# Optimization experiments

Hardware: AMD Instinct MI355X
Metric: run time of the kernel (lower is better)

Reference implementation:

```python
import jax, jax.numpy as jnp
import numpy as np

EPS = 1.1920929e-7  # torch.finfo(float32).eps, default for F.rms_norm
ATTN_SCALE = 0.1
ROPE_BASE = 10000.0


def _rms_norm(x):
    # F.rms_norm over last dim, no learned weight
    return x * jax.lax.rsqrt(jnp.mean(x * x, axis=-1, keepdims=True) + EPS)


def _rotary(x):
    # x: [B, T, H, D]; rotates halves as in the Rotary module
    T, D = x.shape[1], x.shape[3]
    half = D // 2
    inv_freq = 1.0 / (ROPE_BASE ** (jnp.arange(0, D, 2, dtype=jnp.float32) / D))  # [half]
    freqs = jnp.arange(T, dtype=jnp.float32)[:, None] * inv_freq[None, :]          # [T, half]
    cos = jnp.cos(freqs)[None, :, None, :]
    sin = jnp.sin(freqs)[None, :, None, :]
    x1, x2 = x[..., :half], x[..., half:]
    return jnp.concatenate([x1 * cos + x2 * sin, -x1 * sin + x2 * cos], axis=-1)


def setup_inputs() -> dict:
    key = jax.random.key(0)
    ks = jax.random.split(key, 8)
    B, T, dim, H, hd = 2, 2048, 1024, 16, 64
    gate_in = 12
    s = 1.0 / np.sqrt(dim)
    return {
        "x": jax.random.normal(ks[0], (B, T, dim), dtype=jnp.float32),
        "v1": jax.random.normal(ks[1], (B, T, H, hd), dtype=jnp.float32),
        "Wq": jax.random.uniform(ks[2], (dim, dim), jnp.float32, -s, s),
        "Wk": jax.random.uniform(ks[3], (dim, dim), jnp.float32, -s, s),
        "Wv": jax.random.uniform(ks[4], (dim, dim), jnp.float32, -s, s),
        "Wproj": jax.random.uniform(ks[5], (dim, dim), jnp.float32, -s, s),
        "Wg": jax.random.uniform(ks[6], (H, gate_in), jnp.float32,
                                  -1.0 / np.sqrt(gate_in), 1.0 / np.sqrt(gate_in)),
        "lamb": jnp.float32(0.5),
    }


def reference(x, v1, Wq, Wk, Wv, Wproj, Wg, lamb):
    B, T, dim = x.shape
    H, hd = v1.shape[2], v1.shape[3]
    q = (x @ Wq.T).reshape(B, T, H, hd)
    k = (x @ Wk.T).reshape(B, T, H, hd)
    v = (x @ Wv.T).reshape(B, T, H, hd)
    # value-residual mixing
    v = (1.0 - lamb) * v + lamb * v1
    # QK RMSNorm + RoPE
    q = _rotary(_rms_norm(q))
    k = _rotary(_rms_norm(k))
    # causal SDPA with fixed scale
    scores = jnp.einsum('bqhd,bkhd->bhqk', q, k) * ATTN_SCALE
    causal = jnp.tril(jnp.ones((T, T), dtype=bool))
    scores = jnp.where(causal[None, None], scores, jnp.float32(-jnp.inf))
    probs = jax.nn.softmax(scores, axis=-1)
    y = jnp.einsum('bhqk,bkhd->bqhd', probs, v)  # [B, T, H, hd]
    # sigmoid gate from first 12 channels of x
    gate = jax.nn.sigmoid(x[..., :Wg.shape[1]] @ Wg.T)  # [B, T, H]
    y = y * gate[..., None]
    y = y.reshape(B, T, H * hd) @ Wproj.T
    return y
```

## Files before the change

kernel.cpp:

```cpp
#include <hip/hip_runtime.h>
#include <math.h>


#define B_    2
#define T_    2048
#define DIM_  1024
#define H_    16
#define HD_   64
#define NROW  (B_ * T_)
#define EPS_  1.1920929e-07f
#define SCALE_ 0.1f
#define LOG2_10K 13.287712379549449f
#define INV2PI 0.15915494309189535f

typedef unsigned short u16;
typedef unsigned int   u32;
typedef __bf16 bf16x8 __attribute__((ext_vector_type(8)));
typedef __bf16 bf16x2 __attribute__((ext_vector_type(2)));
typedef float  f32x4  __attribute__((ext_vector_type(4)));

__device__ __forceinline__ u16 f2b(float f) {
  u32 u = __float_as_uint(f);
  u += 0x7fffu + ((u >> 16) & 1u);
  return (u16)(u >> 16);
}
__device__ __forceinline__ u32 pk2(float a, float b) {
#if __has_builtin(__builtin_amdgcn_cvt_pk_bf16_f32)
  bf16x2 r = __builtin_amdgcn_cvt_pk_bf16_f32(a, b);
  return __builtin_bit_cast(u32, r);
#else
  return (u32)f2b(a) | ((u32)f2b(b) << 16);
#endif
}
__device__ __forceinline__ void fast_sincos_rev(float rev, float* s, float* c) {
  const float r = rev - floorf(rev);
#if __has_builtin(__builtin_amdgcn_sinf) && __has_builtin(__builtin_amdgcn_cosf)
  *s = __builtin_amdgcn_sinf(r);
  *c = __builtin_amdgcn_cosf(r);
#else
  *s = __sinf(r * 6.283185307179586f);
  *c = __cosf(r * 6.283185307179586f);
#endif
}
#define MFMA16(a,b,c) __builtin_amdgcn_mfma_f32_16x16x32_bf16((a),(b),(c),0,0,0)

typedef const __attribute__((address_space(1))) unsigned char gbuf_t;
typedef __attribute__((address_space(3))) unsigned char lbuf_t;
__device__ __forceinline__ void gload_lds16(const u16* g, unsigned char* l) {
  __builtin_amdgcn_global_load_lds((gbuf_t*)g, (lbuf_t*)l, 16, 0, 0);
}

__global__ __launch_bounds__(256) void convert_all(
    const float* __restrict__ x, const float* __restrict__ Wq,
    const float* __restrict__ Wk, const float* __restrict__ Wv,
    const float* __restrict__ Wp,
    u16* __restrict__ xb, u16* __restrict__ wb ) {
  const int i = blockIdx.x * 256 + threadIdx.x;
  const float* src;
  u16* dst;
  int off;
  if (i < 1048576)       { src = x;  dst = xb;            off = i; }
  else if (i < 1310720)  { src = Wq; dst = wb;            off = i - 1048576; }
  else if (i < 1572864)  { src = Wk; dst = wb + 1048576;  off = i - 1310720; }
  else if (i < 1835008)  { src = Wv; dst = wb + 2097152;  off = i - 1572864; }
  else                   { src = Wp; dst = wb + 3145728;  off = i - 1835008; }
  const float4 f = ((const float4*)src)[off];
  uint2 o;
  o.x = pk2(f.x, f.y);
  o.y = pk2(f.z, f.w);
  ((uint2*)dst)[off] = o;
}

template <bool IS_PROJ>
__global__ __launch_bounds__(256) void gemm_rp(
    const u16* __restrict__ Ab, const u16* __restrict__ Wb,
    u16* __restrict__ qo, u16* __restrict__ ko, u16* __restrict__ vto,
    float* __restrict__ fo, const float* __restrict__ v1,
    const float* __restrict__ lambp) {
  __shared__ __attribute__((aligned(16))) unsigned char sm[49152];
  const int tid  = threadIdx.x;
  const int w    = tid >> 6;
  const int lane = tid & 63;
  const int lo = lane & 15, hi = lane >> 4;
  const int m0 = blockIdx.x << 7;
  const int by = blockIdx.y;
  const int mode = IS_PROJ ? 3 : (by >> 3);
  const int n0 = IS_PROJ ? (by << 7) : ((by & 7) << 7);
  const u16* W = IS_PROJ ? Wb : (Wb + (size_t)mode * (DIM_ * DIM_));

  const int wm = w & 1, wn = w >> 1;

  const u16* agA0 = Ab + (size_t)(m0 + (2 * w + 0) * 16 + lo) * DIM_ + (hi << 3);
  const u16* agA1 = Ab + (size_t)(m0 + (2 * w + 1) * 16 + lo) * DIM_ + (hi << 3);
  const u16* agB0 = W  + (size_t)(n0 + (2 * w + 0) * 16 + lo) * DIM_ + (hi << 3);
  const u16* agB1 = W  + (size_t)(n0 + (2 * w + 1) * 16 + lo) * DIM_ + (hi << 3);

  f32x4 acc[4][4];
#pragma unroll
  for (int i = 0; i < 4; ++i)
#pragma unroll
    for (int j = 0; j < 4; ++j) acc[i][j] = (f32x4){0.f, 0.f, 0.f, 0.f};

  {
    unsigned char* ad0 = sm + (2 * w) * 1024;
    gload_lds16(agA0, ad0);
    gload_lds16(agA1, ad0 + 1024);
    gload_lds16(agB0, ad0 + 8192);
    gload_lds16(agB1, ad0 + 9216);
    agA0 += 32; agA1 += 32; agB0 += 32; agB1 += 32;
    unsigned char* ad1 = sm + 16384 + (2 * w) * 1024;
    gload_lds16(agA0, ad1);
    gload_lds16(agA1, ad1 + 1024);
    gload_lds16(agB0, ad1 + 8192);
    gload_lds16(agB1, ad1 + 9216);
    agA0 += 32; agA1 += 32; agB0 += 32; agB1 += 32;
  }

  int cr = 0;
  int cw = 2;
  for (int kc = 0; kc < DIM_; kc += 32) {
    __builtin_amdgcn_sched_barrier(0);
    if (kc + 32 < DIM_) {
      asm volatile("s_waitcnt vmcnt(4)" ::: "memory");
    } else {
      asm volatile("s_waitcnt vmcnt(0)" ::: "memory");
    }
    __builtin_amdgcn_s_barrier();
    __builtin_amdgcn_sched_barrier(0);
    if (kc + 64 < DIM_) {
      unsigned char* ad = sm + cw * 16384 + (2 * w) * 1024;
      gload_lds16(agA0, ad);
      gload_lds16(agA1, ad + 1024);
      gload_lds16(agB0, ad + 8192);
      gload_lds16(agB1, ad + 9216);
      agA0 += 32; agA1 += 32; agB0 += 32; agB1 += 32;
    }
    const unsigned char* Acur = sm + cr * 16384;
    const unsigned char* Bcur = Acur + 8192;
    bf16x8 bfr[4];
#pragma unroll
    for (int nt = 0; nt < 4; ++nt)
      bfr[nt] = *(const bf16x8*)(Bcur + (((wn * 4 + nt) * 64 + lane) << 4));
#pragma unroll
    for (int mt = 0; mt < 4; ++mt) {
      const bf16x8 af = *(const bf16x8*)(Acur + (((wm * 4 + mt) * 64 + lane) << 4));
#pragma unroll
      for (int nt = 0; nt < 4; ++nt)
        acc[mt][nt] = MFMA16(af, bfr[nt], acc[mt][nt]);
    }
    cr = (cr == 2) ? 0 : cr + 1;
    cw = (cw == 2) ? 0 : cw + 1;
  }

  const int head = (n0 >> 6) + wn;
  if (mode <= 1) {
    u16* C = (mode == 0) ? qo : ko;
    const float if0 = exp2f(-(float)lo * (LOG2_10K / 32.f)) * INV2PI;
    const float if1 = exp2f(-(float)(lo + 16) * (LOG2_10K / 32.f)) * INV2PI;
#pragma unroll
    for (int mt = 0; mt < 4; ++mt)
#pragma unroll
      for (int r = 0; r < 4; ++r) {
        float ss = 0.f;
#pragma unroll
        for (int nt = 0; nt < 4; ++nt) { const float v = acc[mt][nt][r]; ss += v * v; }
        ss += __shfl_xor(ss, 1, 64); ss += __shfl_xor(ss, 2, 64);
        ss += __shfl_xor(ss, 4, 64); ss += __shfl_xor(ss, 8, 64);
        const float scl = rsqrtf(ss * (1.f / 64.f) + EPS_);
        const int row_g = m0 + wm * 64 + mt * 16 + hi * 4 + r;
        const float tpos = (float)(row_g & (T_ - 1));
        float sn0, cs0, sn1, cs1;
        fast_sincos_rev(tpos * if0, &sn0, &cs0);
        fast_sincos_rev(tpos * if1, &sn1, &cs1);
        u16* crow = C + (size_t)row_g * DIM_ + head * HD_;
        const float x10 = acc[mt][0][r] * scl, x11 = acc[mt][1][r] * scl;
        const float x20 = acc[mt][2][r] * scl, x21 = acc[mt][3][r] * scl;
        crow[lo]      = f2b(x10 * cs0 + x20 * sn0);
        crow[16 + lo] = f2b(x11 * cs1 + x21 * sn1);
        crow[32 + lo] = f2b(x20 * cs0 - x10 * sn0);
        crow[48 + lo] = f2b(x21 * cs1 - x11 * sn1);
      }
  } else if (mode == 2) {
    const float lam = lambp[0];
#pragma unroll
    for (int mt = 0; mt < 4; ++mt)
#pragma unroll
      for (int r = 0; r < 4; ++r) {
        const int row_g = m0 + wm * 64 + mt * 16 + hi * 4 + r;
        const int bb = row_g >> 11, tt = row_g & (T_ - 1);
        const int bh = bb * H_ + head;
        const float* v1r = v1 + (size_t)row_g * DIM_ + head * HD_;
#pragma unroll
        for (int nt = 0; nt < 4; ++nt) {
          const int d = nt * 16 + lo;
          const float ov = (1.f - lam) * acc[mt][nt][r] + lam * v1r[d];
          vto[((size_t)(bh * HD_ + d)) * T_ + tt] = f2b(ov);
        }
      }
  } else {
#pragma unroll
    for (int mt = 0; mt < 4; ++mt)
#pragma unroll
      for (int r = 0; r < 4; ++r) {
        const int row_g = m0 + wm * 64 + mt * 16 + hi * 4 + r;
        float* orow = fo + (size_t)row_g * DIM_ + n0 + wn * 64;
#pragma unroll
        for (int nt = 0; nt < 4; ++nt) orow[nt * 16 + lo] = acc[mt][nt][r];
      }
  }
}

__global__ __launch_bounds__(256) void gate_kernel(
    const float* __restrict__ x, const float* __restrict__ Wg,
    float* __restrict__ gate) {
  const int id = blockIdx.x * 256 + threadIdx.x;
  const int n = id >> 4, h = id & 15;
  const float* xr = x + (size_t)n * DIM_;
  const float* wr = Wg + h * 12;
  float s = 0.f;
#pragma unroll
  for (int j = 0; j < 12; ++j) s += xr[j] * wr[j];
  gate[id] = 1.f / (1.f + __expf(-s));
}

__global__ __launch_bounds__(256) void attn3(
    const u16* __restrict__ q, const u16* __restrict__ k, const u16* __restrict__ vt,
    const float* __restrict__ gate, u16* __restrict__ y) {
  __shared__ __attribute__((aligned(16))) unsigned char smem[16384];
  const int tid = threadIdx.x;
  const int wv = tid >> 6, lane = tid & 63, lo = lane & 15, hi = lane >> 4;
  const int idx = blockIdx.x;
  const int qt = 31 - (idx >> 5);
  const int bh = idx & 31;
  const int b = bh >> 4, h = bh & 15;
  const int qb = qt << 6;

  const int qrow = b * T_ + qb + wv * 16 + lo;
  const u16* qp = q + (size_t)qrow * DIM_ + h * HD_;
  const bf16x8 qf0 = *(const bf16x8*)(qp + hi * 8);
  const bf16x8 qf1 = *(const bf16x8*)(qp + 32 + hi * 8);

  f32x4 o[4];
#pragma unroll
  for (int i = 0; i < 4; ++i) o[i] = (f32x4){0.f, 0.f, 0.f, 0.f};
  float lrun = 0.f;

  const int sl = tid & 63, skh = (tid >> 6) & 1, st0 = tid >> 7;
  const int srow = sl & 15, skk = skh * 32 + ((sl >> 4) << 3);
  const u16* kg0 = k + ((size_t)(b * T_ + st0 * 16 + srow)) * DIM_ + h * HD_ + skk;
  const u16* kg1 = kg0 + (size_t)32 * DIM_;
  const u16* vg0 = vt + ((size_t)(bh * HD_ + st0 * 16 + srow)) * T_ + skk;
  const u16* vg1 = vg0 + (size_t)32 * T_;

  uint4 kr0 = *(const uint4*)kg0, kr1 = *(const uint4*)kg1;
  uint4 vr0 = *(const uint4*)vg0, vr1 = *(const uint4*)vg1;

  const int off0 = tid << 4, off1 = (tid + 256) << 4;

  for (int tix = 0; tix <= qt; ++tix) {
    __syncthreads();
    *(uint4*)(smem + off0) = kr0;
    *(uint4*)(smem + off1) = kr1;
    *(uint4*)(smem + 8192 + off0) = vr0;
    *(uint4*)(smem + 8192 + off1) = vr1;
    if (tix < qt) {
      const size_t ko = (size_t)(tix + 1) * 64 * DIM_;
      const size_t vo = (size_t)(tix + 1) * 64;
      kr0 = *(const uint4*)(kg0 + ko); kr1 = *(const uint4*)(kg1 + ko);
      vr0 = *(const uint4*)(vg0 + vo); vr1 = *(const uint4*)(vg1 + vo);
    }
    __syncthreads();

    f32x4 stl[4];
#pragma unroll
    for (int kt = 0; kt < 4; ++kt) stl[kt] = (f32x4){0.f, 0.f, 0.f, 0.f};
    __builtin_amdgcn_s_setprio(1);
#pragma unroll
    for (int kh = 0; kh < 2; ++kh) {
      const bf16x8 qb_ = kh ? qf1 : qf0;
#pragma unroll
      for (int kt = 0; kt < 4; ++kt) {
        const bf16x8 af = *(const bf16x8*)(smem + (((kt * 2 + kh) * 64 + lane) << 4));
        stl[kt] = MFMA16(af, qb_, stl[kt]);
      }
    }
    __builtin_amdgcn_s_setprio(0);
    const bool diag = (tix == qt);
    float ps = 0.f;
#pragma unroll
    for (int kt = 0; kt < 4; ++kt)
#pragma unroll
      for (int r = 0; r < 4; ++r) {
        float s = stl[kt][r] * SCALE_;
        if (diag && (kt * 16 + hi * 4 + r > wv * 16 + lo)) s = -3e38f;
        const float e = __expf(s);
        stl[kt][r] = e;
        ps += e;
      }
    ps += __shfl_xor(ps, 16, 64);
    ps += __shfl_xor(ps, 32, 64);
    lrun += ps;

    u32 pkv[4][2];
#pragma unroll
    for (int kt = 0; kt < 4; ++kt) {
      pkv[kt][0] = pk2(stl[kt][0], stl[kt][1]);
      pkv[kt][1] = pk2(stl[kt][2], stl[kt][3]);
    }
#pragma unroll
    for (int kh = 0; kh < 2; ++kh) {
      uint4 w4;
      u32* w4p = (u32*)&w4;
#pragma unroll
      for (int wd = 0; wd < 4; ++wd) {
        const int src = (2 * (hi & 1) + (wd >> 1)) * 16 + lo;
        const u32 a  = (u32)__shfl((int)pkv[2 * kh][wd & 1], src, 64);
        const u32 bb = (u32)__shfl((int)pkv[2 * kh + 1][wd & 1], src, 64);
        w4p[wd] = (hi < 2) ? a : bb;
      }
      const bf16x8 pf = __builtin_bit_cast(bf16x8, w4);
      __builtin_amdgcn_s_setprio(1);
#pragma unroll
      for (int dt = 0; dt < 4; ++dt) {
        const bf16x8 vf = *(const bf16x8*)(smem + 8192 + (((dt * 2 + kh) * 64 + lane) << 4));
        o[dt] = MFMA16(vf, pf, o[dt]);
      }
      __builtin_amdgcn_s_setprio(0);
    }
  }

  const float inv = gate[(size_t)qrow * H_ + h] / lrun;
  u16* yrow = y + (size_t)qrow * DIM_ + h * HD_;
#pragma unroll
  for (int dt = 0; dt < 4; ++dt) {
    ushort4 pq;
    pq.x = f2b(o[dt][0] * inv); pq.y = f2b(o[dt][1] * inv);
    pq.z = f2b(o[dt][2] * inv); pq.w = f2b(o[dt][3] * inv);
    *(ushort4*)(yrow + dt * 16 + hi * 4) = pq;
  }
}

extern "C" void kernel_launch(void* const* d_in, const int* in_sizes, int n_in,
                              void* d_out, int out_size, void* d_ws, size_t ws_size,
                              hipStream_t stream) {
  const float* x    = (const float*)d_in[0];
  const float* v1   = (const float*)d_in[1];
  const float* Wq   = (const float*)d_in[2];
  const float* Wk   = (const float*)d_in[3];
  const float* Wv   = (const float*)d_in[4];
  const float* Wp   = (const float*)d_in[5];
  const float* Wg   = (const float*)d_in[6];
  const float* lamb = (const float*)d_in[7];

  const size_t NX = (size_t)NROW * DIM_;
  const size_t NW = (size_t)DIM_ * DIM_;

  u16* q  = (u16*)d_ws;
  u16* k  = q + NX;
  u16* vt = k + NX;
  u16* xb = vt + NX;
  u16* wb = xb + NX;
  float* gate = (float*)(wb + 4 * NW);

  const dim3 bb(256);

  convert_all<<<dim3(8192), bb, 0, stream>>>(x, Wq, Wk, Wv, Wp, xb, wb);
  gemm_rp<false><<<dim3(NROW / 128, 24), bb, 0, stream>>>(
      xb, wb, q, k, vt, nullptr, v1, lamb);
  gate_kernel<<<dim3(NROW * H_ / 256), bb, 0, stream>>>(x, Wg, gate);
  attn3<<<dim3(B_ * H_ * (T_ / 64)), bb, 0, stream>>>(q, k, vt, gate, q);
  gemm_rp<true><<<dim3(NROW / 128, 8), bb, 0, stream>>>(
      q, wb + 3 * NW, nullptr, nullptr, nullptr, (float*)d_out, nullptr, nullptr);
}
```

Before: 221.3 us.

## Triple-buffer attention K/V via direct-to-LDS loads and XCD-aware block remap

The attention kernel now streams K/V tiles with direct global-to-LDS loads into a three-stage ring buffer. It prefetches two tiles ahead and uses explicit vmcnt waits with a single barrier per iteration, replacing register staging and two barriers. Both GEMM and attention grids are flattened and remapped so consecutive blocks on the same XCD share A rows or the same batch-head, aiming for better L2 locality. LDS use in attention triples to 48KB, which may reduce occupancy.

New measurement: 221.0 us. No clear change (-0.1%).

```diff
diff --git a/kernel.cpp b/kernel.cpp
--- a/kernel.cpp
+++ b/kernel.cpp
@@ -82,8 +82,11 @@
   const int w    = tid >> 6;
   const int lane = tid & 63;
   const int lo = lane & 15, hi = lane >> 4;
-  const int m0 = blockIdx.x << 7;
-  const int by = blockIdx.y;
+  const int raw = blockIdx.x;
+  const int xcd = raw & 7;
+  const int jj  = raw >> 3;
+  const int m0 = (xcd * 4 + (jj & 3)) << 7;
+  const int by = jj >> 2;
   const int mode = IS_PROJ ? 3 : (by >> 3);
   const int n0 = IS_PROJ ? (by << 7) : ((by & 7) << 7);
   const u16* W = IS_PROJ ? Wb : (Wb + (size_t)mode * (DIM_ * DIM_));
@@ -226,12 +229,14 @@
 __global__ __launch_bounds__(256) void attn3(
     const u16* __restrict__ q, const u16* __restrict__ k, const u16* __restrict__ vt,
     const float* __restrict__ gate, u16* __restrict__ y) {
-  __shared__ __attribute__((aligned(16))) unsigned char smem[16384];
+  __shared__ __attribute__((aligned(16))) unsigned char smem[49152];
   const int tid = threadIdx.x;
   const int wv = tid >> 6, lane = tid & 63, lo = lane & 15, hi = lane >> 4;
-  const int idx = blockIdx.x;
-  const int qt = 31 - (idx >> 5);
-  const int bh = idx & 31;
+  const int raw = blockIdx.x;
+  const int xcd = raw & 7;
+  const int jj  = raw >> 3;
+  const int qt = 31 - (jj >> 2);
+  const int bh = xcd * 4 + (jj & 3);
   const int b = bh >> 4, h = bh & 15;
   const int qb = qt << 6;
 
@@ -251,25 +256,44 @@
   const u16* kg1 = kg0 + (size_t)32 * DIM_;
   const u16* vg0 = vt + ((size_t)(bh * HD_ + st0 * 16 + srow)) * T_ + skk;
   const u16* vg1 = vg0 + (size_t)32 * T_;
-
-  uint4 kr0 = *(const uint4*)kg0, kr1 = *(const uint4*)kg1;
-  uint4 vr0 = *(const uint4*)vg0, vr1 = *(const uint4*)vg1;
-
-  const int off0 = tid << 4, off1 = (tid + 256) << 4;
-
+  const int wub = (tid >> 6) << 10;
+
+  {
+    gload_lds16(kg0, smem + wub);
+    gload_lds16(kg1, smem + 4096 + wub);
+    gload_lds16(vg0, smem + 8192 + wub);
+    gload_lds16(vg1, smem + 12288 + wub);
+    const int t1 = (qt >= 1) ? 1 : 0;
+    const size_t ko = (size_t)t1 * 64 * DIM_;
+    const size_t vo = (size_t)t1 * 64;
+    unsigned char* b1 = smem + 16384;
+    gload_lds16(kg0 + ko, b1 + wub);
+    gload_lds16(kg1 + ko, b1 + 4096 + wub);
+    gload_lds16(vg0 + vo, b1 + 8192 + wub);
+    gload_lds16(vg1 + vo, b1 + 12288 + wub);
+  }
+
+  int sr = 0, sw = 2;
   for (int tix = 0; tix <= qt; ++tix) {
-    __syncthreads();
-    *(uint4*)(smem + off0) = kr0;
-    *(uint4*)(smem + off1) = kr1;
-    *(uint4*)(smem + 8192 + off0) = vr0;
-    *(uint4*)(smem + 8192 + off1) = vr1;
+    __builtin_amdgcn_sched_barrier(0);
     if (tix < qt) {
-      const size_t ko = (size_t)(tix + 1) * 64 * DIM_;
-      const size_t vo = (size_t)(tix + 1) * 64;
-      kr0 = *(const uint4*)(kg0 + ko); kr1 = *(const uint4*)(kg1 + ko);
-      vr0 = *(const uint4*)(vg0 + vo); vr1 = *(const uint4*)(vg1 + vo);
-    }
-    __syncthreads();
+      asm volatile("s_waitcnt vmcnt(4)" ::: "memory");
+    } else {
+      asm volatile("s_waitcnt vmcnt(0)" ::: "memory");
+    }
+    __builtin_amdgcn_s_barrier();
+    __builtin_amdgcn_sched_barrier(0);
+    if (tix + 2 <= qt) {
+      const size_t ko = (size_t)(tix + 2) * 64 * DIM_;
+      const size_t vo = (size_t)(tix + 2) * 64;
+      unsigned char* base = smem + sw * 16384;
+      gload_lds16(kg0 + ko, base + wub);
+      gload_lds16(kg1 + ko, base + 4096 + wub);
+      gload_lds16(vg0 + vo, base + 8192 + wub);
+      gload_lds16(vg1 + vo, base + 12288 + wub);
+    }
+    const unsigned char* kb = smem + sr * 16384;
+    const unsigned char* vb = kb + 8192;
 
     f32x4 stl[4];
 #pragma unroll
@@ -280,7 +304,7 @@
       const bf16x8 qb_ = kh ? qf1 : qf0;
 #pragma unroll
       for (int kt = 0; kt < 4; ++kt) {
-        const bf16x8 af = *(const bf16x8*)(smem + (((kt * 2 + kh) * 64 + lane) << 4));
+        const bf16x8 af = *(const bf16x8*)(kb + (((kt * 2 + kh) * 64 + lane) << 4));
         stl[kt] = MFMA16(af, qb_, stl[kt]);
       }
     }
@@ -322,11 +346,13 @@
       __builtin_amdgcn_s_setprio(1);
 #pragma unroll
       for (int dt = 0; dt < 4; ++dt) {
-        const bf16x8 vf = *(const bf16x8*)(smem + 8192 + (((dt * 2 + kh) * 64 + lane) << 4));
+        const bf16x8 vf = *(const bf16x8*)(vb + (((dt * 2 + kh) * 64 + lane) << 4));
         o[dt] = MFMA16(vf, pf, o[dt]);
       }
       __builtin_amdgcn_s_setprio(0);
     }
+    sr = (sr == 2) ? 0 : sr + 1;
+    sw = (sw == 2) ? 0 : sw + 1;
   }
 
   const float inv = gate[(size_t)qrow * H_ + h] / lrun;
@@ -365,10 +391,10 @@
   const dim3 bb(256);
 
   convert_all<<<dim3(8192), bb, 0, stream>>>(x, Wq, Wk, Wv, Wp, xb, wb);
-  gemm_rp<false><<<dim3(NROW / 128, 24), bb, 0, stream>>>(
+  gemm_rp<false><<<dim3(768), bb, 0, stream>>>(
       xb, wb, q, k, vt, nullptr, v1, lamb);
   gate_kernel<<<dim3(NROW * H_ / 256), bb, 0, stream>>>(x, Wg, gate);
-  attn3<<<dim3(B_ * H_ * (T_ / 64)), bb, 0, stream>>>(q, k, vt, gate, q);
-  gemm_rp<true><<<dim3(NROW / 128, 8), bb, 0, stream>>>(
+  attn3<<<dim3(1024), bb, 0, stream>>>(q, k, vt, gate, q);
+  gemm_rp<true><<<dim3(256), bb, 0, stream>>>(
       q, wb + 3 * NW, nullptr, nullptr, nullptr, (float*)d_out, nullptr, nullptr);
 }
```
